# Kernel optimization log

Hardware: AMD Instinct MI355X
Metric: run time of the kernel (lower is better)

The kernel has to match this reference:

```python
import jax, jax.numpy as jnp
import numpy as np

EPS = 1e-12  # torch F.normalize default eps

def _l2norm(x, axis=-1):
    n = jnp.linalg.norm(x, axis=axis, keepdims=True)
    return x / jnp.maximum(n, EPS)

def setup_inputs() -> dict:
    key = jax.random.key(0)
    k1, k2 = jax.random.split(key)
    query = jax.random.normal(k1, (65536, 512), dtype=jnp.float32)
    prototypes = jax.random.normal(k2, (64, 512), dtype=jnp.float32)
    return {"query": query, "prototypes": prototypes, "k": 3}

def reference(query, prototypes, k):
    # cosine similarity between queries and prototypes: [B, P]
    sim = jnp.einsum('bd,pd->bp', _l2norm(query), _l2norm(prototypes))
    k = min(int(k), prototypes.shape[0])
    weights, indices = jax.lax.top_k(sim, k)          # [B, k]
    retrieved = prototypes[indices]                   # [B, k, D]
    w = jax.nn.softmax(weights, axis=1)               # [B, k]
    return jnp.einsum('bkd,bk->bd', retrieved, w)     # [B, D]
```

## Files before the change

kernel.cpp:

```cpp
#include <hip/hip_runtime.h>
#include <math.h>

#define DIM 512
#define NP  64
#define RPB 64
#define BK  64
#define NCH 8
#define TAU 4e-5f
#define LISTCAP 8192
#define RFB 128

#define WS_PTW   0
#define WS_BHI   131072
#define WS_BLO   196608
#define WS_INV64 262144
#define WS_CNT   262656
#define WS_LIST  262784

typedef __attribute__((ext_vector_type(8))) short bf16x8;
typedef __attribute__((ext_vector_type(4))) float f32x4;

__device__ __forceinline__ unsigned short f2bf(float f) {
  const unsigned int u = __float_as_uint(f);
  return (unsigned short)((u + 0x7FFFu + ((u >> 16) & 1u)) >> 16);
}
__device__ __forceinline__ float bf2f(unsigned short h) {
  return __uint_as_float(((unsigned int)h) << 16);
}

__device__ __forceinline__ void gload_lds16(const void* g, void* l) {
  __builtin_amdgcn_global_load_lds(
      (const __attribute__((address_space(1))) void*)g,
      (__attribute__((address_space(3))) void*)l, 16, 0, 0);
}

__device__ __forceinline__ void ins4f(float v, int idx, float& v0, float& v1,
                                      float& v2, float& v3, int& j0, int& j1,
                                      int& j2, int& j3) {
  const bool b0 = v > v0, b1 = v > v1, b2 = v > v2, b3 = v > v3;
  v3 = b2 ? v2 : (b3 ? v : v3);  j3 = b2 ? j2 : (b3 ? idx : j3);
  v2 = b1 ? v1 : (b2 ? v : v2);  j2 = b1 ? j1 : (b2 ? idx : j2);
  v1 = b0 ? v0 : (b1 ? v : v1);  j1 = b0 ? j0 : (b1 ? idx : j1);
  v0 = b0 ? v  : v0;             j0 = b0 ? idx : j0;
}

__device__ __forceinline__ void ins3d(double v, int idx, double& b0, double& b1,
                                      double& b2, int& k0, int& k1, int& k2) {
  const bool c0 = v > b0, c1 = v > b1, c2 = v > b2;
  b2 = c1 ? b1 : (c2 ? v : b2);  k2 = c1 ? k1 : (c2 ? idx : k2);
  b1 = c0 ? b0 : (c1 ? v : b1);  k1 = c0 ? k0 : (c1 ? idx : k1);
  b0 = c0 ? v  : b0;             k0 = c0 ? idx : k0;
}

__global__ __launch_bounds__(256) void prep_kernel(
    const float* __restrict__ protos, float* __restrict__ ptw,
    double* __restrict__ inv64, int* __restrict__ cnt) {
  if (blockIdx.x == 0 && threadIdx.x == 0) *cnt = 0;
  const int p = (blockIdx.x * 256 + threadIdx.x) >> 6;
  const int lane = threadIdx.x & 63;
  if (p >= NP) return;
  const float4* pr = (const float4*)(protos + (size_t)p * DIM);
  const float4 a = pr[lane * 2];
  const float4 b = pr[lane * 2 + 1];
  double ss = (double)a.x * a.x + (double)a.y * a.y + (double)a.z * a.z +
              (double)a.w * a.w + (double)b.x * b.x + (double)b.y * b.y +
              (double)b.z * b.z + (double)b.w * b.w;
#pragma unroll
  for (int m = 1; m < 64; m <<= 1) ss += __shfl_xor(ss, m);
  const double inv = 1.0 / fmax(sqrt(ss), 1e-12);
  if (lane == 0) inv64[p] = inv;
  const float v[8] = {a.x, a.y, a.z, a.w, b.x, b.y, b.z, b.w};
#pragma unroll
  for (int e = 0; e < 8; ++e)
    ptw[(size_t)(lane * 8 + e) * NP + p] = v[e];
}

__global__ __launch_bounds__(64) void prep_frag_kernel(
    const float* __restrict__ protos, const double* __restrict__ inv64,
    unsigned short* __restrict__ bhi, unsigned short* __restrict__ blo) {
  const int ks = blockIdx.x >> 2;
  const int pt = blockIdx.x & 3;
  const int l = threadIdx.x;
  const int p = pt * 16 + (l & 15);
  const int k0 = ks * 32 + (l >> 4) * 8;
  const double inv = inv64[p];
  const size_t base = ((size_t)(ks * 4 + pt) * 64 + l) * 8;
#pragma unroll
  for (int e = 0; e < 8; ++e) {
    const float v = (float)((double)protos[(size_t)p * DIM + k0 + e] * inv);
    const unsigned short h = f2bf(v);
    bhi[base + e] = h;
    blo[base + e] = f2bf(v - bf2f(h));
  }
}

__global__ __launch_bounds__(256) void sim_kernel(
    const float* __restrict__ query, const float* __restrict__ protos,
    const unsigned short* __restrict__ bhi_u, const unsigned short* __restrict__ blo_u,
    float* __restrict__ out, int* __restrict__ cnt, int* __restrict__ list) {
  __shared__ __align__(16) float Abuf[2][RPB * BK];
  __shared__ float4 wiS[4][16];

  const int t = threadIdx.x;
  const int wid = t >> 6;
  const int l = t & 63;
  const int lr = l & 15;
  const int lg = l >> 4;
  const int row0 = blockIdx.x * RPB;
  const int wr0 = row0 + wid * 16;

  const int srow_i = l >> 4;
  const int sbyte = (l & 15) * 16;

  auto stage = [&](int bufi, int cc) {
#pragma unroll
    for (int i = 0; i < 4; ++i) {
      const int r0 = wid * 16 + i * 4;
      const int row = r0 + srow_i;
      const char* src = (const char*)query +
          ((size_t)(row0 + row) * DIM + cc * BK) * 4 +
          (sbyte ^ ((row & 7) << 4));
      gload_lds16(src, &Abuf[bufi][r0 * BK]);
    }
  };

  const bf16x8* bhp = (const bf16x8*)bhi_u;
  const bf16x8* blp = (const bf16x8*)blo_u;

  f32x4 acc[4] = {};
  float ss = 0.f;

  bf16x8 hbuf[2][4], lbuf[2][4];
#pragma unroll
  for (int s = 0; s < 2; ++s)
#pragma unroll
    for (int j = 0; j < 4; ++j) {
      hbuf[s][j] = bhp[(size_t)(s * 4 + j) * 64 + l];
      lbuf[s][j] = blp[(size_t)(s * 4 + j) * 64 + l];
    }

  stage(0, 0);
  __syncthreads();

  const int swz = (lr & 7) << 4;

  for (int c = 0; c < NCH; ++c) {
    const int cur = c & 1;
    if (c + 1 < NCH) stage(cur ^ 1, c + 1);

    const char* ab = (const char*)&Abuf[cur][0];
#pragma unroll
    for (int s = 0; s < 2; ++s) {
      const int ks = c * 2 + s;
      const int rbase = (wid * 16 + lr) * 256 + s * 128;
      const float4 a0 = *(const float4*)(ab + rbase + ((lg * 32) ^ swz));
      const float4 a1 = *(const float4*)(ab + rbase + ((lg * 32 + 16) ^ swz));
      bf16x8 ahi, alo;
      const float av[8] = {a0.x, a0.y, a0.z, a0.w, a1.x, a1.y, a1.z, a1.w};
#pragma unroll
      for (int i = 0; i < 8; ++i) {
        const unsigned int u = __float_as_uint(av[i]);
        const unsigned short h = (unsigned short)(u >> 16);
        ahi[i] = (short)h;
        alo[i] = (short)f2bf(av[i] - bf2f(h));
        ss += av[i] * av[i];
      }
#pragma unroll
      for (int pt = 0; pt < 4; ++pt) {
        acc[pt] = __builtin_amdgcn_mfma_f32_16x16x32_bf16(ahi, hbuf[s][pt], acc[pt], 0, 0, 0);
        acc[pt] = __builtin_amdgcn_mfma_f32_16x16x32_bf16(ahi, lbuf[s][pt], acc[pt], 0, 0, 0);
        acc[pt] = __builtin_amdgcn_mfma_f32_16x16x32_bf16(alo, hbuf[s][pt], acc[pt], 0, 0, 0);
      }
      if (ks + 2 < 16) {
#pragma unroll
        for (int j = 0; j < 4; ++j) {
          hbuf[s][j] = bhp[(size_t)((ks + 2) * 4 + j) * 64 + l];
          lbuf[s][j] = blp[(size_t)((ks + 2) * 4 + j) * 64 + l];
        }
      }
    }
    __syncthreads();
  }

  ss += __shfl_xor(ss, 16);
  ss += __shfl_xor(ss, 32);

#pragma unroll
  for (int e = 0; e < 4; ++e) {
    float v0 = -1e30f, v1 = -1e30f, v2 = -1e30f, v3 = -1e30f;
    int j0 = 0, j1 = 0, j2 = 0, j3 = 0;
#pragma unroll
    for (int pt = 0; pt < 4; ++pt)
      ins4f(acc[pt][e], pt * 16 + lr, v0, v1, v2, v3, j0, j1, j2, j3);
#pragma unroll
    for (int m = 1; m <= 8; m <<= 1) {
      const float p0 = __shfl_xor(v0, m), p1 = __shfl_xor(v1, m);
      const float p2 = __shfl_xor(v2, m), p3 = __shfl_xor(v3, m);
      const int q0 = __shfl_xor(j0, m), q1 = __shfl_xor(j1, m);
      const int q2 = __shfl_xor(j2, m), q3 = __shfl_xor(j3, m);
      ins4f(p0, q0, v0, v1, v2, v3, j0, j1, j2, j3);
      ins4f(p1, q1, v0, v1, v2, v3, j0, j1, j2, j3);
      ins4f(p2, q2, v0, v1, v2, v3, j0, j1, j2, j3);
      ins4f(p3, q3, v0, v1, v2, v3, j0, j1, j2, j3);
    }
    const float ssr = __shfl(ss, lg * 4 + e);
    if (lr == e) {
      const int row = lg * 4 + e;
      const float qi = 1.0f / fmaxf(sqrtf(ssr), 1e-12f);
      const float s0 = v0 * qi, s1 = v1 * qi, s2 = v2 * qi, s3 = v3 * qi;
      const float e1 = expf(s1 - s0), e2 = expf(s2 - s0);
      const float inv = 1.0f / (1.0f + e1 + e2);
      wiS[wid][row] = make_float4(inv, e1 * inv, e2 * inv,
                                  __int_as_float(j0 | (j1 << 6) | (j2 << 12)));
      if (s2 - s3 < TAU) {
        const int pos = atomicAdd(cnt, 1);
        if (pos < LISTCAP) list[pos] = wr0 + row;
      }
    }
  }

#pragma unroll 2
  for (int r = 0; r < 16; ++r) {
    const float4 wi = wiS[wid][r];
    const int pack = __float_as_int(wi.w);
    const int i0 = pack & 63, i1 = (pack >> 6) & 63, i2 = (pack >> 12) & 63;
    const float* p0 = protos + (size_t)i0 * DIM;
    const float* p1 = protos + (size_t)i1 * DIM;
    const float* p2 = protos + (size_t)i2 * DIM;
    float* orow = out + (size_t)(wr0 + r) * DIM;
#pragma unroll
    for (int h = 0; h < 2; ++h) {
      const int col = h * 256 + l * 4;
      const float4 x = *(const float4*)(p0 + col);
      const float4 y = *(const float4*)(p1 + col);
      const float4 z = *(const float4*)(p2 + col);
      float4 res;
      res.x = wi.x * x.x + wi.y * y.x + wi.z * z.x;
      res.y = wi.x * x.y + wi.y * y.y + wi.z * z.y;
      res.z = wi.x * x.z + wi.y * y.z + wi.z * z.z;
      res.w = wi.x * x.w + wi.y * y.w + wi.z * z.w;
      *(float4*)(orow + col) = res;
    }
  }
}

__global__ __launch_bounds__(256) void refine_kernel(
    const float* __restrict__ query, const float* __restrict__ protos,
    const float* __restrict__ ptw, const double* __restrict__ inv64,
    const int* __restrict__ cnt, const int* __restrict__ list,
    float* __restrict__ out) {
  const int n = min(*cnt, LISTCAP);
  const int lane = threadIdx.x & 63;
  const int gw = blockIdx.x * 4 + (threadIdx.x >> 6);

  for (int i = gw; i < n; i += RFB * 4) {
    const int row = list[i];
    const float* q = query + (size_t)row * DIM;
    double a0 = 0.0, a1 = 0.0, a2 = 0.0, a3 = 0.0;
    float qs = 0.f;
#pragma unroll 4
    for (int k = 0; k < DIM; k += 4) {
      const float4 qv = *(const float4*)(q + k);
      a0 = fma((double)qv.x, (double)ptw[(size_t)(k + 0) * NP + lane], a0);
      a1 = fma((double)qv.y, (double)ptw[(size_t)(k + 1) * NP + lane], a1);
      a2 = fma((double)qv.z, (double)ptw[(size_t)(k + 2) * NP + lane], a2);
      a3 = fma((double)qv.w, (double)ptw[(size_t)(k + 3) * NP + lane], a3);
      qs += qv.x * qv.x + qv.y * qv.y + qv.z * qv.z + qv.w * qv.w;
    }
    const double sim = (a0 + a1 + a2 + a3) * inv64[lane];

    double b0 = sim, b1 = -1e300, b2 = -1e300;
    int k0 = lane, k1 = 0, k2 = 0;
#pragma unroll
    for (int m = 1; m <= 32; m <<= 1) {
      const double p0 = __shfl_xor(b0, m), p1 = __shfl_xor(b1, m),
                   p2 = __shfl_xor(b2, m);
      const int q0 = __shfl_xor(k0, m), q1 = __shfl_xor(k1, m),
                q2 = __shfl_xor(k2, m);
      ins3d(p0, q0, b0, b1, b2, k0, k1, k2);
      ins3d(p1, q1, b0, b1, b2, k0, k1, k2);
      ins3d(p2, q2, b0, b1, b2, k0, k1, k2);
    }
    const double qi = 1.0 / fmax(sqrt((double)qs), 1e-12);
    const double s0 = b0 * qi, s1 = b1 * qi, s2 = b2 * qi;
    const double e1 = exp(s1 - s0), e2 = exp(s2 - s0);
    const double inv = 1.0 / (1.0 + e1 + e2);
    const double w0 = inv, w1 = e1 * inv, w2 = e2 * inv;
    const float* p0r = protos + (size_t)k0 * DIM;
    const float* p1r = protos + (size_t)k1 * DIM;
    const float* p2r = protos + (size_t)k2 * DIM;
#pragma unroll
    for (int u = 0; u < 2; ++u) {
      const int col = u * 256 + lane * 4;
      const float4 x = *(const float4*)(p0r + col);
      const float4 y = *(const float4*)(p1r + col);
      const float4 z = *(const float4*)(p2r + col);
      float4 res;
      res.x = (float)(w0 * x.x + w1 * y.x + w2 * z.x);
      res.y = (float)(w0 * x.y + w1 * y.y + w2 * z.y);
      res.z = (float)(w0 * x.z + w1 * y.z + w2 * z.z);
      res.w = (float)(w0 * x.w + w1 * y.w + w2 * z.w);
      *(float4*)(out + (size_t)row * DIM + col) = res;
    }
  }
}

extern "C" void kernel_launch(void* const* d_in, const int* in_sizes, int n_in,
                              void* d_out, int out_size, void* d_ws, size_t ws_size,
                              hipStream_t stream) {
  const float* query = (const float*)d_in[0];
  const float* protos = (const float*)d_in[1];
  float* out = (float*)d_out;
  float* ptw = (float*)((char*)d_ws + WS_PTW);
  unsigned short* bhi = (unsigned short*)((char*)d_ws + WS_BHI);
  unsigned short* blo = (unsigned short*)((char*)d_ws + WS_BLO);
  double* inv64 = (double*)((char*)d_ws + WS_INV64);
  int* cnt = (int*)((char*)d_ws + WS_CNT);
  int* list = (int*)((char*)d_ws + WS_LIST);

  const int nrows = in_sizes[0] / DIM;

  hipLaunchKernelGGL(prep_kernel, dim3(16), dim3(256), 0, stream,
                     protos, ptw, inv64, cnt);
  hipLaunchKernelGGL(prep_frag_kernel, dim3(64), dim3(64), 0, stream,
                     protos, inv64, bhi, blo);
  hipLaunchKernelGGL(sim_kernel, dim3(nrows / RPB), dim3(256), 0, stream,
                     query, protos, bhi, blo, out, cnt, list);
  hipLaunchKernelGGL(refine_kernel, dim3(RFB), dim3(256), 0, stream,
                     query, protos, ptw, inv64, cnt, list, out);
}
```

Before: 109.9 us.

## Split prototypes across waves with register-resident B and 4-deep query staging

Each wave now owns 16 prototypes and keeps all of its bf16 hi/lo prototype fragments in registers for the whole K loop, instead of streaming them from global memory per k-step. All four waves share every query row of the block. Query chunks are staged through a 4-buffer LDS ring of 32-column slices, with explicit vmcnt waits and a barrier per chunk. The per-row top-4 is now merged across waves through shared memory and finished by wave 0. This removes the repeated B-fragment loads but raises register pressure, makes each wave convert every query row, and adds cross-wave LDS merging.

```diff
diff --git a/kernel.cpp b/kernel.cpp
--- a/kernel.cpp
+++ b/kernel.cpp
@@ -3,9 +3,6 @@
 
 #define DIM 512
 #define NP  64
-#define RPB 64
-#define BK  64
-#define NCH 8
 #define TAU 4e-5f
 #define LISTCAP 8192
 #define RFB 128
@@ -98,136 +95,154 @@
     const float* __restrict__ query, const float* __restrict__ protos,
     const unsigned short* __restrict__ bhi_u, const unsigned short* __restrict__ blo_u,
     float* __restrict__ out, int* __restrict__ cnt, int* __restrict__ list) {
-  __shared__ __align__(16) float Abuf[2][RPB * BK];
-  __shared__ float4 wiS[4][16];
+  __shared__ __align__(16) float Abuf[4][64 * 32];
+  __shared__ float4 topV[4][64];
+  __shared__ int4   topJ[4][64];
+  __shared__ float  ssS[64];
+  __shared__ float4 wiS[64];
 
   const int t = threadIdx.x;
   const int wid = t >> 6;
   const int l = t & 63;
   const int lr = l & 15;
   const int lg = l >> 4;
-  const int row0 = blockIdx.x * RPB;
-  const int wr0 = row0 + wid * 16;
-
-  const int srow_i = l >> 4;
-  const int sbyte = (l & 15) * 16;
-
-  auto stage = [&](int bufi, int cc) {
-#pragma unroll
-    for (int i = 0; i < 4; ++i) {
-      const int r0 = wid * 16 + i * 4;
-      const int row = r0 + srow_i;
-      const char* src = (const char*)query +
-          ((size_t)(row0 + row) * DIM + cc * BK) * 4 +
-          (sbyte ^ ((row & 7) << 4));
-      gload_lds16(src, &Abuf[bufi][r0 * BK]);
-    }
-  };
+  const int row0 = blockIdx.x * 64;
 
   const bf16x8* bhp = (const bf16x8*)bhi_u;
   const bf16x8* blp = (const bf16x8*)blo_u;
+  bf16x8 Bh[16], Bl[16];
+#pragma unroll
+  for (int c = 0; c < 16; ++c) {
+    Bh[c] = bhp[(size_t)(c * 4 + wid) * 64 + l];
+    Bl[c] = blp[(size_t)(c * 4 + wid) * 64 + l];
+  }
+
+  const int srow = l >> 3;
+  const int sg = l & 7;
+  auto stage = [&](int cc) {
+    const int bi = cc & 3;
+#pragma unroll
+    for (int i = 0; i < 2; ++i) {
+      const int rowl = wid * 16 + i * 8 + srow;
+      const char* src = (const char*)query +
+          (size_t)(row0 + rowl) * 2048 + cc * 128 + ((sg ^ (rowl & 7)) << 4);
+      gload_lds16(src, (char*)&Abuf[bi][0] + (wid * 16 + i * 8) * 128);
+    }
+  };
 
   f32x4 acc[4] = {};
-  float ss = 0.f;
-
-  bf16x8 hbuf[2][4], lbuf[2][4];
-#pragma unroll
-  for (int s = 0; s < 2; ++s)
-#pragma unroll
-    for (int j = 0; j < 4; ++j) {
-      hbuf[s][j] = bhp[(size_t)(s * 4 + j) * 64 + l];
-      lbuf[s][j] = blp[(size_t)(s * 4 + j) * 64 + l];
-    }
-
-  stage(0, 0);
+  float ss[4] = {0.f, 0.f, 0.f, 0.f};
+
+  stage(0); stage(1); stage(2);
+  const int g0 = lg * 2;
+  const int sw = lr & 7;
+
+#define SIM_CHUNK(C, NV)                                                      \
+  {                                                                           \
+    asm volatile("s_waitcnt vmcnt(" #NV ")" ::: "memory");                    \
+    __builtin_amdgcn_sched_barrier(0);                                        \
+    __builtin_amdgcn_s_barrier();                                             \
+    if ((C) + 3 < 16) stage((C) + 3);                                         \
+    const char* ab = (const char*)&Abuf[(C) & 3][0];                          \
+    _Pragma("unroll")                                                         \
+    for (int rg = 0; rg < 4; ++rg) {                                          \
+      const int rl = rg * 16 + lr;                                            \
+      const float4 a0 = *(const float4*)(ab + rl * 128 + ((g0 ^ sw) << 4));   \
+      const float4 a1 = *(const float4*)(ab + rl * 128 + (((g0 + 1) ^ sw) << 4)); \
+      const float av[8] = {a0.x, a0.y, a0.z, a0.w, a1.x, a1.y, a1.z, a1.w};   \
+      bf16x8 ahi, alo;                                                        \
+      _Pragma("unroll")                                                       \
+      for (int i = 0; i < 8; ++i) {                                           \
+        const unsigned int u = __float_as_uint(av[i]);                        \
+        const unsigned short h = (unsigned short)(u >> 16);                   \
+        ahi[i] = (short)h;                                                    \
+        alo[i] = (short)f2bf(av[i] - bf2f(h));                                \
+        ss[rg] += av[i] * av[i];                                              \
+      }                                                                       \
+      acc[rg] = __builtin_amdgcn_mfma_f32_16x16x32_bf16(ahi, Bh[(C)], acc[rg], 0, 0, 0); \
+      acc[rg] = __builtin_amdgcn_mfma_f32_16x16x32_bf16(ahi, Bl[(C)], acc[rg], 0, 0, 0); \
+      acc[rg] = __builtin_amdgcn_mfma_f32_16x16x32_bf16(alo, Bh[(C)], acc[rg], 0, 0, 0); \
+    }                                                                         \
+  }
+
+  SIM_CHUNK(0, 4)  SIM_CHUNK(1, 4)  SIM_CHUNK(2, 4)  SIM_CHUNK(3, 4)
+  SIM_CHUNK(4, 4)  SIM_CHUNK(5, 4)  SIM_CHUNK(6, 4)  SIM_CHUNK(7, 4)
+  SIM_CHUNK(8, 4)  SIM_CHUNK(9, 4)  SIM_CHUNK(10, 4) SIM_CHUNK(11, 4)
+  SIM_CHUNK(12, 4) SIM_CHUNK(13, 4) SIM_CHUNK(14, 2) SIM_CHUNK(15, 0)
+#undef SIM_CHUNK
+
+#pragma unroll
+  for (int rg = 0; rg < 4; ++rg) {
+    ss[rg] += __shfl_xor(ss[rg], 16);
+    ss[rg] += __shfl_xor(ss[rg], 32);
+  }
+  if (wid == 0 && l < 16) {
+#pragma unroll
+    for (int rg = 0; rg < 4; ++rg) ssS[rg * 16 + l] = ss[rg];
+  }
+
+#pragma unroll
+  for (int rg = 0; rg < 4; ++rg) {
+#pragma unroll
+    for (int e = 0; e < 4; ++e) {
+      float v0 = acc[rg][e], v1 = -1e30f, v2 = -1e30f, v3 = -1e30f;
+      int j0 = wid * 16 + lr, j1 = 0, j2 = 0, j3 = 0;
+#pragma unroll
+      for (int m = 1; m <= 8; m <<= 1) {
+        const float p0 = __shfl_xor(v0, m), p1 = __shfl_xor(v1, m);
+        const float p2 = __shfl_xor(v2, m), p3 = __shfl_xor(v3, m);
+        const int q0 = __shfl_xor(j0, m), q1 = __shfl_xor(j1, m);
+        const int q2 = __shfl_xor(j2, m), q3 = __shfl_xor(j3, m);
+        ins4f(p0, q0, v0, v1, v2, v3, j0, j1, j2, j3);
+        ins4f(p1, q1, v0, v1, v2, v3, j0, j1, j2, j3);
+        ins4f(p2, q2, v0, v1, v2, v3, j0, j1, j2, j3);
+        ins4f(p3, q3, v0, v1, v2, v3, j0, j1, j2, j3);
+      }
+      if (lr == 0) {
+        const int r = rg * 16 + lg * 4 + e;
+        topV[wid][r] = make_float4(v0, v1, v2, v3);
+        topJ[wid][r] = make_int4(j0, j1, j2, j3);
+      }
+    }
+  }
   __syncthreads();
 
-  const int swz = (lr & 7) << 4;
-
-  for (int c = 0; c < NCH; ++c) {
-    const int cur = c & 1;
-    if (c + 1 < NCH) stage(cur ^ 1, c + 1);
-
-    const char* ab = (const char*)&Abuf[cur][0];
-#pragma unroll
-    for (int s = 0; s < 2; ++s) {
-      const int ks = c * 2 + s;
-      const int rbase = (wid * 16 + lr) * 256 + s * 128;
-      const float4 a0 = *(const float4*)(ab + rbase + ((lg * 32) ^ swz));
-      const float4 a1 = *(const float4*)(ab + rbase + ((lg * 32 + 16) ^ swz));
-      bf16x8 ahi, alo;
-      const float av[8] = {a0.x, a0.y, a0.z, a0.w, a1.x, a1.y, a1.z, a1.w};
-#pragma unroll
-      for (int i = 0; i < 8; ++i) {
-        const unsigned int u = __float_as_uint(av[i]);
-        const unsigned short h = (unsigned short)(u >> 16);
-        ahi[i] = (short)h;
-        alo[i] = (short)f2bf(av[i] - bf2f(h));
-        ss += av[i] * av[i];
-      }
-#pragma unroll
-      for (int pt = 0; pt < 4; ++pt) {
-        acc[pt] = __builtin_amdgcn_mfma_f32_16x16x32_bf16(ahi, hbuf[s][pt], acc[pt], 0, 0, 0);
-        acc[pt] = __builtin_amdgcn_mfma_f32_16x16x32_bf16(ahi, lbuf[s][pt], acc[pt], 0, 0, 0);
-        acc[pt] = __builtin_amdgcn_mfma_f32_16x16x32_bf16(alo, hbuf[s][pt], acc[pt], 0, 0, 0);
-      }
-      if (ks + 2 < 16) {
-#pragma unroll
-        for (int j = 0; j < 4; ++j) {
-          hbuf[s][j] = bhp[(size_t)((ks + 2) * 4 + j) * 64 + l];
-          lbuf[s][j] = blp[(size_t)((ks + 2) * 4 + j) * 64 + l];
-        }
-      }
-    }
-    __syncthreads();
-  }
-
-  ss += __shfl_xor(ss, 16);
-  ss += __shfl_xor(ss, 32);
-
-#pragma unroll
-  for (int e = 0; e < 4; ++e) {
+  if (wid == 0) {
+    const int r = l;
     float v0 = -1e30f, v1 = -1e30f, v2 = -1e30f, v3 = -1e30f;
     int j0 = 0, j1 = 0, j2 = 0, j3 = 0;
 #pragma unroll
-    for (int pt = 0; pt < 4; ++pt)
-      ins4f(acc[pt][e], pt * 16 + lr, v0, v1, v2, v3, j0, j1, j2, j3);
-#pragma unroll
-    for (int m = 1; m <= 8; m <<= 1) {
-      const float p0 = __shfl_xor(v0, m), p1 = __shfl_xor(v1, m);
-      const float p2 = __shfl_xor(v2, m), p3 = __shfl_xor(v3, m);
-      const int q0 = __shfl_xor(j0, m), q1 = __shfl_xor(j1, m);
-      const int q2 = __shfl_xor(j2, m), q3 = __shfl_xor(j3, m);
-      ins4f(p0, q0, v0, v1, v2, v3, j0, j1, j2, j3);
-      ins4f(p1, q1, v0, v1, v2, v3, j0, j1, j2, j3);
-      ins4f(p2, q2, v0, v1, v2, v3, j0, j1, j2, j3);
-      ins4f(p3, q3, v0, v1, v2, v3, j0, j1, j2, j3);
-    }
-    const float ssr = __shfl(ss, lg * 4 + e);
-    if (lr == e) {
-      const int row = lg * 4 + e;
-      const float qi = 1.0f / fmaxf(sqrtf(ssr), 1e-12f);
-      const float s0 = v0 * qi, s1 = v1 * qi, s2 = v2 * qi, s3 = v3 * qi;
-      const float e1 = expf(s1 - s0), e2 = expf(s2 - s0);
-      const float inv = 1.0f / (1.0f + e1 + e2);
-      wiS[wid][row] = make_float4(inv, e1 * inv, e2 * inv,
-                                  __int_as_float(j0 | (j1 << 6) | (j2 << 12)));
-      if (s2 - s3 < TAU) {
-        const int pos = atomicAdd(cnt, 1);
-        if (pos < LISTCAP) list[pos] = wr0 + row;
-      }
-    }
-  }
+    for (int w = 0; w < 4; ++w) {
+      const float4 tv = topV[w][r];
+      const int4 tj = topJ[w][r];
+      ins4f(tv.x, tj.x, v0, v1, v2, v3, j0, j1, j2, j3);
+      ins4f(tv.y, tj.y, v0, v1, v2, v3, j0, j1, j2, j3);
+      ins4f(tv.z, tj.z, v0, v1, v2, v3, j0, j1, j2, j3);
+      ins4f(tv.w, tj.w, v0, v1, v2, v3, j0, j1, j2, j3);
+    }
+    const float qi = 1.0f / fmaxf(sqrtf(ssS[r]), 1e-12f);
+    const float s0 = v0 * qi, s1 = v1 * qi, s2 = v2 * qi, s3 = v3 * qi;
+    const float e1 = expf(s1 - s0), e2 = expf(s2 - s0);
+    const float inv = 1.0f / (1.0f + e1 + e2);
+    wiS[r] = make_float4(inv, e1 * inv, e2 * inv,
+                         __int_as_float(j0 | (j1 << 6) | (j2 << 12)));
+    if (s2 - s3 < TAU) {
+      const int pos = atomicAdd(cnt, 1);
+      if (pos < LISTCAP) list[pos] = row0 + r;
+    }
+  }
+  __syncthreads();
 
 #pragma unroll 2
   for (int r = 0; r < 16; ++r) {
-    const float4 wi = wiS[wid][r];
+    const int row = wid * 16 + r;
+    const float4 wi = wiS[row];
     const int pack = __float_as_int(wi.w);
     const int i0 = pack & 63, i1 = (pack >> 6) & 63, i2 = (pack >> 12) & 63;
     const float* p0 = protos + (size_t)i0 * DIM;
     const float* p1 = protos + (size_t)i1 * DIM;
     const float* p2 = protos + (size_t)i2 * DIM;
-    float* orow = out + (size_t)(wr0 + r) * DIM;
+    float* orow = out + (size_t)(row0 + row) * DIM;
 #pragma unroll
     for (int h = 0; h < 2; ++h) {
       const int col = h * 256 + l * 4;
@@ -324,7 +339,7 @@
                      protos, ptw, inv64, cnt);
   hipLaunchKernelGGL(prep_frag_kernel, dim3(64), dim3(64), 0, stream,
                      protos, inv64, bhi, blo);
-  hipLaunchKernelGGL(sim_kernel, dim3(nrows / RPB), dim3(256), 0, stream,
+  hipLaunchKernelGGL(sim_kernel, dim3(nrows / 64), dim3(256), 0, stream,
                      query, protos, bhi, blo, out, cnt, list);
   hipLaunchKernelGGL(refine_kernel, dim3(RFB), dim3(256), 0, stream,
                      query, protos, ptw, inv64, cnt, list, out);
```

Measured after the change: 407.2 us. +270.4%, slower.

## Make sim kernel per-wave staged with triple-buffered LDS and no block barriers

Applied to the files above, without the earlier changes.

Each wave now stages only its own 16 query rows into a private three-slot LDS ring, 32 columns per step. Progress is tracked with explicit vmcnt waits instead of block-wide __syncthreads, and the 16-step loop is fully unrolled by macro with prefetch two steps ahead for both the query tiles and the B fragments. The goal is to remove block synchronisation stalls and keep more loads in flight. It relies on a hand-picked vmcnt count matching the real number of outstanding loads. Per-wave LDS reads without any barrier also carry a correctness risk.

```diff
diff --git a/kernel.cpp b/kernel.cpp
--- a/kernel.cpp
+++ b/kernel.cpp
@@ -3,9 +3,6 @@
 
 #define DIM 512
 #define NP  64
-#define RPB 64
-#define BK  64
-#define NCH 8
 #define TAU 4e-5f
 #define LISTCAP 8192
 #define RFB 128
@@ -98,29 +95,25 @@
     const float* __restrict__ query, const float* __restrict__ protos,
     const unsigned short* __restrict__ bhi_u, const unsigned short* __restrict__ blo_u,
     float* __restrict__ out, int* __restrict__ cnt, int* __restrict__ list) {
-  __shared__ __align__(16) float Abuf[2][RPB * BK];
-  __shared__ float4 wiS[4][16];
+  __shared__ __align__(16) float Abuf[4][3][512];
+  __shared__ float4 wiSw[4][16];
 
   const int t = threadIdx.x;
   const int wid = t >> 6;
   const int l = t & 63;
   const int lr = l & 15;
   const int lg = l >> 4;
-  const int row0 = blockIdx.x * RPB;
+  const int row0 = blockIdx.x * 64;
   const int wr0 = row0 + wid * 16;
 
-  const int srow_i = l >> 4;
-  const int sbyte = (l & 15) * 16;
-
-  auto stage = [&](int bufi, int cc) {
-#pragma unroll
-    for (int i = 0; i < 4; ++i) {
-      const int r0 = wid * 16 + i * 4;
-      const int row = r0 + srow_i;
+  const int sgswz = ((l & 7) ^ (l >> 3)) << 4;
+  const int srow = l >> 3;
+  auto stage = [&](int cc) {
+#pragma unroll
+    for (int i = 0; i < 2; ++i) {
       const char* src = (const char*)query +
-          ((size_t)(row0 + row) * DIM + cc * BK) * 4 +
-          (sbyte ^ ((row & 7) << 4));
-      gload_lds16(src, &Abuf[bufi][r0 * BK]);
+          (size_t)(wr0 + i * 8 + srow) * 2048 + cc * 128 + sgswz;
+      gload_lds16(src, (char*)&Abuf[wid][cc % 3][0] + i * 1024);
     }
   };
 
@@ -129,58 +122,65 @@
 
   f32x4 acc[4] = {};
   float ss = 0.f;
-
-  bf16x8 hbuf[2][4], lbuf[2][4];
-#pragma unroll
-  for (int s = 0; s < 2; ++s)
-#pragma unroll
-    for (int j = 0; j < 4; ++j) {
-      hbuf[s][j] = bhp[(size_t)(s * 4 + j) * 64 + l];
-      lbuf[s][j] = blp[(size_t)(s * 4 + j) * 64 + l];
-    }
-
-  stage(0, 0);
-  __syncthreads();
-
-  const int swz = (lr & 7) << 4;
-
-  for (int c = 0; c < NCH; ++c) {
-    const int cur = c & 1;
-    if (c + 1 < NCH) stage(cur ^ 1, c + 1);
-
-    const char* ab = (const char*)&Abuf[cur][0];
-#pragma unroll
-    for (int s = 0; s < 2; ++s) {
-      const int ks = c * 2 + s;
-      const int rbase = (wid * 16 + lr) * 256 + s * 128;
-      const float4 a0 = *(const float4*)(ab + rbase + ((lg * 32) ^ swz));
-      const float4 a1 = *(const float4*)(ab + rbase + ((lg * 32 + 16) ^ swz));
-      bf16x8 ahi, alo;
-      const float av[8] = {a0.x, a0.y, a0.z, a0.w, a1.x, a1.y, a1.z, a1.w};
-#pragma unroll
-      for (int i = 0; i < 8; ++i) {
-        const unsigned int u = __float_as_uint(av[i]);
-        const unsigned short h = (unsigned short)(u >> 16);
-        ahi[i] = (short)h;
-        alo[i] = (short)f2bf(av[i] - bf2f(h));
-        ss += av[i] * av[i];
-      }
-#pragma unroll
-      for (int pt = 0; pt < 4; ++pt) {
-        acc[pt] = __builtin_amdgcn_mfma_f32_16x16x32_bf16(ahi, hbuf[s][pt], acc[pt], 0, 0, 0);
-        acc[pt] = __builtin_amdgcn_mfma_f32_16x16x32_bf16(ahi, lbuf[s][pt], acc[pt], 0, 0, 0);
-        acc[pt] = __builtin_amdgcn_mfma_f32_16x16x32_bf16(alo, hbuf[s][pt], acc[pt], 0, 0, 0);
-      }
-      if (ks + 2 < 16) {
-#pragma unroll
-        for (int j = 0; j < 4; ++j) {
-          hbuf[s][j] = bhp[(size_t)((ks + 2) * 4 + j) * 64 + l];
-          lbuf[s][j] = blp[(size_t)((ks + 2) * 4 + j) * 64 + l];
-        }
-      }
-    }
-    __syncthreads();
-  }
+  bf16x8 Bh[2][4], Bl[2][4];
+
+  stage(0);
+#pragma unroll
+  for (int pt = 0; pt < 4; ++pt) {
+    Bh[0][pt] = bhp[(size_t)(0 * 4 + pt) * 64 + l];
+    Bl[0][pt] = blp[(size_t)(0 * 4 + pt) * 64 + l];
+  }
+  __builtin_amdgcn_sched_barrier(0);
+  stage(1);
+#pragma unroll
+  for (int pt = 0; pt < 4; ++pt) {
+    Bh[1][pt] = bhp[(size_t)(1 * 4 + pt) * 64 + l];
+    Bl[1][pt] = blp[(size_t)(1 * 4 + pt) * 64 + l];
+  }
+
+  const int g0 = lg * 2;
+  const int sw = lr & 7;
+  const char* abase = (const char*)&Abuf[wid][0][0];
+
+#define SIM_CHUNK(C, NV)                                                      \
+  {                                                                           \
+    asm volatile("s_waitcnt vmcnt(" #NV ")" ::: "memory");                    \
+    __builtin_amdgcn_sched_barrier(0);                                        \
+    if ((C) + 2 < 16) stage((C) + 2);                                         \
+    const char* ab = abase + ((C) % 3) * 2048;                                \
+    const float4 a0 = *(const float4*)(ab + lr * 128 + ((g0 ^ sw) << 4));     \
+    const float4 a1 = *(const float4*)(ab + lr * 128 + (((g0 + 1) ^ sw) << 4)); \
+    const float av[8] = {a0.x, a0.y, a0.z, a0.w, a1.x, a1.y, a1.z, a1.w};     \
+    bf16x8 ahi, alo;                                                          \
+    _Pragma("unroll")                                                         \
+    for (int i = 0; i < 8; ++i) {                                             \
+      const unsigned int u = __float_as_uint(av[i]);                          \
+      const unsigned short h = (unsigned short)(u >> 16);                     \
+      ahi[i] = (short)h;                                                      \
+      alo[i] = (short)f2bf(av[i] - bf2f(h));                                  \
+      ss += av[i] * av[i];                                                    \
+    }                                                                         \
+    const int bb = (C) & 1;                                                   \
+    _Pragma("unroll")                                                         \
+    for (int pt = 0; pt < 4; ++pt) {                                          \
+      acc[pt] = __builtin_amdgcn_mfma_f32_16x16x32_bf16(ahi, Bh[bb][pt], acc[pt], 0, 0, 0); \
+      acc[pt] = __builtin_amdgcn_mfma_f32_16x16x32_bf16(ahi, Bl[bb][pt], acc[pt], 0, 0, 0); \
+      acc[pt] = __builtin_amdgcn_mfma_f32_16x16x32_bf16(alo, Bh[bb][pt], acc[pt], 0, 0, 0); \
+    }                                                                         \
+    if ((C) + 2 < 16) {                                                       \
+      _Pragma("unroll")                                                       \
+      for (int pt = 0; pt < 4; ++pt) {                                        \
+        Bh[bb][pt] = bhp[(size_t)(((C) + 2) * 4 + pt) * 64 + l];              \
+        Bl[bb][pt] = blp[(size_t)(((C) + 2) * 4 + pt) * 64 + l];              \
+      }                                                                       \
+    }                                                                         \
+  }
+
+  SIM_CHUNK(0, 10)  SIM_CHUNK(1, 10)  SIM_CHUNK(2, 10)  SIM_CHUNK(3, 10)
+  SIM_CHUNK(4, 10)  SIM_CHUNK(5, 10)  SIM_CHUNK(6, 10)  SIM_CHUNK(7, 10)
+  SIM_CHUNK(8, 10)  SIM_CHUNK(9, 10)  SIM_CHUNK(10, 10) SIM_CHUNK(11, 10)
+  SIM_CHUNK(12, 10) SIM_CHUNK(13, 10) SIM_CHUNK(14, 10) SIM_CHUNK(15, 0)
+#undef SIM_CHUNK
 
   ss += __shfl_xor(ss, 16);
   ss += __shfl_xor(ss, 32);
@@ -204,14 +204,14 @@
       ins4f(p3, q3, v0, v1, v2, v3, j0, j1, j2, j3);
     }
     const float ssr = __shfl(ss, lg * 4 + e);
-    if (lr == e) {
+    if (lr == 0) {
       const int row = lg * 4 + e;
       const float qi = 1.0f / fmaxf(sqrtf(ssr), 1e-12f);
       const float s0 = v0 * qi, s1 = v1 * qi, s2 = v2 * qi, s3 = v3 * qi;
       const float e1 = expf(s1 - s0), e2 = expf(s2 - s0);
       const float inv = 1.0f / (1.0f + e1 + e2);
-      wiS[wid][row] = make_float4(inv, e1 * inv, e2 * inv,
-                                  __int_as_float(j0 | (j1 << 6) | (j2 << 12)));
+      wiSw[wid][row] = make_float4(inv, e1 * inv, e2 * inv,
+                                   __int_as_float(j0 | (j1 << 6) | (j2 << 12)));
       if (s2 - s3 < TAU) {
         const int pos = atomicAdd(cnt, 1);
         if (pos < LISTCAP) list[pos] = wr0 + row;
@@ -221,7 +221,7 @@
 
 #pragma unroll 2
   for (int r = 0; r < 16; ++r) {
-    const float4 wi = wiS[wid][r];
+    const float4 wi = wiSw[wid][r];
     const int pack = __float_as_int(wi.w);
     const int i0 = pack & 63, i1 = (pack >> 6) & 63, i2 = (pack >> 12) & 63;
     const float* p0 = protos + (size_t)i0 * DIM;
@@ -324,7 +324,7 @@
                      protos, ptw, inv64, cnt);
   hipLaunchKernelGGL(prep_frag_kernel, dim3(64), dim3(64), 0, stream,
                      protos, inv64, bhi, blo);
-  hipLaunchKernelGGL(sim_kernel, dim3(nrows / RPB), dim3(256), 0, stream,
+  hipLaunchKernelGGL(sim_kernel, dim3(nrows / 64), dim3(256), 0, stream,
                      query, protos, bhi, blo, out, cnt, list);
   hipLaunchKernelGGL(refine_kernel, dim3(RFB), dim3(256), 0, stream,
                      query, protos, ptw, inv64, cnt, list, out);
```

New measurement: 112.0 us. No clear change (+1.9%).
